# Kernel optimization log

Hardware: AMD Instinct MI355X
Metric: run time of the kernel (lower is better)

## Reference

```python
import jax, jax.numpy as jnp
import numpy as np

HEADS = 8
DIM_HEAD = 64
SCALE = DIM_HEAD ** -0.5


def setup_inputs() -> dict:
    key = jax.random.key(0)
    k1, k2, k3 = jax.random.split(key, 3)
    b, dim, n = 4, 256, 2048
    hidden = HEADS * DIM_HEAD  # 512
    x = jax.random.normal(k1, (b, dim, n), dtype=jnp.float32)
    # Conv1d kernel-size-1 weights are pointwise linear maps over channels.
    w_qkv = jax.random.normal(k2, (3 * hidden, dim), dtype=jnp.float32) * (dim ** -0.5)
    w_out = jax.random.normal(k3, (dim, hidden), dtype=jnp.float32) * (hidden ** -0.5)
    b_out = jnp.zeros((dim,), dtype=jnp.float32)
    return {"x": x, "w_qkv": w_qkv, "w_out": w_out, "b_out": b_out}


def reference(x, w_qkv, w_out, b_out):
    b, dim, n = x.shape
    hidden = w_out.shape[1]
    # pointwise conv1d == channel matmul: [3h, dim] x [b, dim, n] -> [b, 3h, n]
    qkv = jnp.einsum('oi,bin->bon', w_qkv, x)
    q, k, v = jnp.split(qkv, 3, axis=1)
    # b (h c) n -> b h c n
    reshape = lambda t: t.reshape(b, HEADS, DIM_HEAD, n)
    q, k, v = reshape(q) * SCALE, reshape(k), reshape(v)
    sim = jnp.einsum('bhdi,bhdj->bhij', q, k)          # [b, h, n, n]
    attn = jax.nn.softmax(sim, axis=-1)
    out = jnp.einsum('bhij,bhdj->bhid', attn, v)        # [b, h, n, d]
    # b h n d -> b (h d) n
    out = out.transpose(0, 1, 3, 2).reshape(b, hidden, n)
    return jnp.einsum('oi,bin->bon', w_out, out) + b_out[None, :, None]
```

## Files before the change

### kernel.cpp

```cpp
#include <hip/hip_runtime.h>
#include <stdint.h>

#define SEQ  2048
#define DIMC 256
#define HID  512
#define NH   8
#define DH   64

typedef __attribute__((ext_vector_type(8))) short bf16x8;
typedef __attribute__((ext_vector_type(4))) float f32x4;
typedef __attribute__((ext_vector_type(16))) float f32x16;
typedef __attribute__((ext_vector_type(2))) unsigned uint2v;
typedef __attribute__((address_space(1))) const uint32_t guint_t;
typedef __attribute__((address_space(3))) uint32_t luint_t;

__device__ __forceinline__ void gld16(const void* g, void* l) {
  __builtin_amdgcn_global_load_lds((guint_t*)g, (luint_t*)l, 16, 0, 0);
}

__device__ __forceinline__ void barrier_raw() {
  asm volatile("" ::: "memory");
  __builtin_amdgcn_s_barrier();
  asm volatile("" ::: "memory");
}
#define WAITVM(n) asm volatile("s_waitcnt vmcnt(" #n ")" ::: "memory")

__device__ __forceinline__ unsigned short f2bf(float f) {
  union { float f; uint32_t u; } v; v.f = f;
  return (unsigned short)((v.u + 0x7FFFu + ((v.u >> 16) & 1u)) >> 16);
}

__device__ __forceinline__ uint32_t fbits(float f) {
  union { float f; uint32_t u; } v; v.f = f; return v.u;
}
__device__ __forceinline__ float ffrombits(uint32_t u) {
  union { uint32_t u; float f; } v; v.u = u; return v.f;
}

__device__ __forceinline__ uint32_t cvtpk(float a, float b) {
  uint32_t r;
  asm("v_cvt_pk_bf16_f32 %0, %1, %2" : "=v"(r) : "v"(a), "v"(b));
  return r;
}

__device__ __forceinline__ void swap32(uint32_t& a, uint32_t& b) {
#if __has_builtin(__builtin_amdgcn_permlane32_swap)
  uint2v r = __builtin_amdgcn_permlane32_swap(a, b, false, false);
  a = r[0]; b = r[1];
#else
  uint32_t aw = __shfl_xor(a, 32);
  uint32_t bw = __shfl_xor(b, 32);
  bool lo = (threadIdx.x & 32) == 0;
  uint32_t an = lo ? a : bw;
  uint32_t bn = lo ? aw : b;
  a = an; b = bn;
#endif
}

__global__ __launch_bounds__(256) void prep_kernel(
    const float* __restrict__ x, const float* __restrict__ wqkv,
    const float* __restrict__ wout,
    unsigned short* __restrict__ wqkv_b, unsigned short* __restrict__ wout_b,
    unsigned short* __restrict__ xT) {
  __shared__ float tile[64][65];
  int blk = blockIdx.x;
  int t = threadIdx.x;
  if (blk < 384) {
    int idx = blk * 1024 + t * 4;
    float4 v = *(const float4*)(wqkv + idx);
    float s = ((idx >> 8) < HID) ? 0.18033688011112042f : 1.0f;
    ushort4 o;
    o.x = f2bf(v.x * s); o.y = f2bf(v.y * s);
    o.z = f2bf(v.z * s); o.w = f2bf(v.w * s);
    *(ushort4*)(wqkv_b + idx) = o;
    return;
  }
  if (blk < 512) {
    int idx = (blk - 384) * 1024 + t * 4;
    float4 v = *(const float4*)(wout + idx);
    ushort4 o;
    o.x = f2bf(v.x); o.y = f2bf(v.y); o.z = f2bf(v.z); o.w = f2bf(v.w);
    *(ushort4*)(wout_b + idx) = o;
    return;
  }
  int tid = blk - 512;
  int b  = tid >> 7;
  int r  = tid & 127;
  int i0 = (r >> 5) * 64;
  int n0 = (r & 31) * 64;
  const float* xb = x + (size_t)b * DIMC * SEQ;
  int tn = t & 15, ti = t >> 4;
#pragma unroll
  for (int j = 0; j < 4; j++) {
    int il = ti + j * 16;
    float4 v = *(const float4*)(xb + (size_t)(i0 + il) * SEQ + n0 + tn * 4);
    tile[il][tn*4+0] = v.x; tile[il][tn*4+1] = v.y;
    tile[il][tn*4+2] = v.z; tile[il][tn*4+3] = v.w;
  }
  __syncthreads();
  unsigned short* xTb = xT + (size_t)b * SEQ * DIMC;
#pragma unroll
  for (int j = 0; j < 4; j++) {
    int nl = ti + j * 16;
    int i4 = tn * 4;
    uint2 pk;
    pk.x = (uint32_t)f2bf(tile[i4+0][nl]) | ((uint32_t)f2bf(tile[i4+1][nl]) << 16);
    pk.y = (uint32_t)f2bf(tile[i4+2][nl]) | ((uint32_t)f2bf(tile[i4+3][nl]) << 16);
    *(uint2*)(xTb + (size_t)(n0 + nl) * DIMC + i0 + i4) = pk;
  }
}

__global__ __launch_bounds__(256, 3) void qkv_gemm(
    const unsigned short* __restrict__ wq, const unsigned short* __restrict__ xT,
    unsigned short* __restrict__ Qs, unsigned short* __restrict__ Ks,
    unsigned short* __restrict__ Vt) {
  __shared__ unsigned short lds[32768];
  int id = blockIdx.x + 12 * blockIdx.y + 192 * blockIdx.z;
  int xcd = id & 7, wg = id >> 3;
  int pair = xcd * 8 + wg / 12;
  int o0 = (wg % 12) * 128;
  int n0 = (pair & 15) * 128;
  int b  = pair >> 4;
  int t  = threadIdx.x;
  int wv = t >> 6, l = t & 63, l15 = l & 15, q = l >> 4;
  int wm = (wv & 1) * 64, wn = (wv >> 1) * 64;
  f32x4 acc[4][4];
#pragma unroll
  for (int i = 0; i < 4; i++)
#pragma unroll
    for (int j = 0; j < 4; j++) acc[i][j] = (f32x4){0.f, 0.f, 0.f, 0.f};
  const unsigned short* Ag = wq + (size_t)o0 * DIMC;
  const unsigned short* Bg = xT + ((size_t)b * SEQ + n0) * DIMC;
  int lrow8 = l >> 3, lcol = l & 7;

  auto stage = [&](int kk, int buf) {
    unsigned short* la = lds + (buf << 14);
    unsigned short* lb = la + 8192;
    int k0 = kk * 64;
#pragma unroll
    for (int c0 = 0; c0 < 4; c0++) {
      int c = wv * 4 + c0;
      int row = c * 8 + lrow8;
      int sg = lcol ^ (row & 7);
      gld16(Ag + (size_t)row * DIMC + k0 + sg * 8, la + c * 512);
      gld16(Bg + (size_t)row * DIMC + k0 + sg * 8, lb + c * 512);
    }
  };

  stage(0, 0);
  for (int kk = 0; kk < 4; kk++) {
    int cur = kk & 1;
    WAITVM(0);
    barrier_raw();
    if (kk < 3) stage(kk + 1, cur ^ 1);
    unsigned short* la = lds + (cur << 14);
    unsigned short* lb = la + 8192;
#pragma unroll
    for (int kh = 0; kh < 2; kh++) {
      bf16x8 af[4], bfr[4];
#pragma unroll
      for (int mt = 0; mt < 4; mt++) {
        int row = wm + mt*16 + l15;
        af[mt] = *(const bf16x8*)(la + row*64 + ((kh*4 + q) ^ (row & 7)) * 8);
      }
#pragma unroll
      for (int nt = 0; nt < 4; nt++) {
        int row = wn + nt*16 + l15;
        bfr[nt] = *(const bf16x8*)(lb + row*64 + ((kh*4 + q) ^ (row & 7)) * 8);
      }
#pragma unroll
      for (int mt = 0; mt < 4; mt++)
#pragma unroll
        for (int nt = 0; nt < 4; nt++)
          acc[mt][nt] = __builtin_amdgcn_mfma_f32_16x16x32_bf16(af[mt], bfr[nt], acc[mt][nt], 0, 0, 0);
    }
  }
  barrier_raw();
  int seg3 = o0 >> 9;
  int h0   = (o0 & 511) >> 6;
  if (seg3 == 2) {
#pragma unroll
    for (int mt = 0; mt < 4; mt++)
#pragma unroll
      for (int nt = 0; nt < 4; nt++)
#pragma unroll
        for (int r = 0; r < 4; r++) {
          int ol = wm + mt * 16 + q * 4 + r;
          int nn = wn + nt * 16 + l15;
          lds[ol * 136 + nn] = f2bf(acc[mt][nt][r]);
        }
    __syncthreads();
#pragma unroll
    for (int i = 0; i < 8; i++) {
      int idx = i * 256 + t;
      int ol  = idx >> 4;
      int nnb = (idx & 15) * 8;
      uint4 v = *(const uint4*)(lds + ol * 136 + nnb);
      int h = h0 + (ol >> 6), d = ol & 63;
      *(uint4*)(Vt + (((size_t)b * NH + h) * DH + d) * SEQ + n0 + nnb) = v;
    }
  } else {
    unsigned short* dst = (seg3 == 0) ? Qs : Ks;
#pragma unroll
    for (int mt = 0; mt < 4; mt++)
#pragma unroll
      for (int nt = 0; nt < 4; nt++)
#pragma unroll
        for (int r = 0; r < 4; r++) {
          int ol = wm + mt * 16 + q * 4 + r;
          int nn = wn + nt * 16 + l15;
          lds[nn * 136 + ol] = f2bf(acc[mt][nt][r]);
        }
    __syncthreads();
#pragma unroll
    for (int i = 0; i < 8; i++) {
      int idx = i * 256 + t;
      int nn  = idx >> 4;
      int olb = (idx & 15) * 8;
      uint4 v = *(const uint4*)(lds + nn * 136 + olb);
      int h = h0 + (olb >> 6), d = olb & 63;
      *(uint4*)(dst + (((size_t)b * NH + h) * SEQ + n0 + nn) * DH + d) = v;
    }
  }
}

__global__ __launch_bounds__(512, 4) void attn_kernel(
    const unsigned short* __restrict__ Qs, const unsigned short* __restrict__ Ks,
    const unsigned short* __restrict__ Vt, unsigned short* __restrict__ AO) {
  __shared__ unsigned short KVs[16384];
  __shared__ float Lc[256];
  int id = blockIdx.x;
  int s  = id >> 3;
  int bh = (id & 7) * 4 + (s & 3);
  int q0 = (s >> 2) * 128;
  int b = bh >> 3, h = bh & 7;
  int t = threadIdx.x;
  int w = t >> 6, l = t & 63, l31 = l & 31, lh = l >> 5;
  int cg = w & 1, qg = w >> 1;
  const unsigned short* Qg = Qs + ((size_t)bh * SEQ + q0 + qg * 32) * DH;
  bf16x8 qb[4];
#pragma unroll
  for (int kc = 0; kc < 4; kc++)
    qb[kc] = *(const bf16x8*)(Qg + l31 * DH + kc*16 + lh*8);
  f32x16 oacc[2];
  float lsum = 0.f;
#pragma unroll
  for (int dt = 0; dt < 2; dt++)
#pragma unroll
    for (int r = 0; r < 16; r++) oacc[dt][r] = 0.f;

  int which = w >> 1, half = w & 1;
  const unsigned short* sgp[2];
  unsigned short* dst0;
  size_t step;
  if (which < 2) {
    const unsigned short* Ksrc = Ks + ((size_t)bh * SEQ + which * 1024) * DH;
#pragma unroll
    for (int gi = 0; gi < 2; gi++) {
      int g = half * 2 + gi;
      int kr = g * 8 + (l >> 3);
      sgp[gi] = Ksrc + (size_t)kr * DH + ((l & 7) ^ (kr & 7)) * 8;
    }
    dst0 = (unsigned short*)KVs + which * 2048 + half * 1024;
    step = (size_t)32 * DH;
  } else {
    const unsigned short* Vsrc = Vt + (size_t)bh * DH * SEQ + (which - 2) * 1024;
#pragma unroll
    for (int gi = 0; gi < 2; gi++) {
      int g = half * 2 + gi;
      int r = g * 8 + (l >> 3);
      int u = (l & 7) ^ (r & 7);
      int d = (u >> 2) * 32 + r;
      int j = u & 3;
      sgp[gi] = Vsrc + (size_t)d * SEQ + j * 8;
    }
    dst0 = (unsigned short*)KVs + 4096 + (which - 2) * 2048 + half * 1024;
    step = 32;
  }

  auto stage = [&](int it2, int buf) {
    size_t off = (size_t)it2 * step;
    unsigned short* dstb = dst0 + buf * 8192;
    gld16(sgp[0] + off, dstb);
    gld16(sgp[1] + off, dstb + 512);
  };

  stage(0, 0);
  for (int it = 0; it < 32; it++) {
    int cur = it & 1;
    WAITVM(0);
    barrier_raw();
    if (it < 31) stage(it + 1, cur ^ 1);
    const unsigned short* Kst = KVs + cur * 8192 + cg * 2048;
    const unsigned short* Vst = KVs + cur * 8192 + 4096 + cg * 2048;
    f32x16 st;
#pragma unroll
    for (int r = 0; r < 16; r++) st[r] = 0.f;
    __builtin_amdgcn_s_setprio(1);
#pragma unroll
    for (int kc = 0; kc < 4; kc++) {
      bf16x8 kf = *(const bf16x8*)(Kst + l31 * 64 + ((kc*2 + lh) ^ (l31 & 7)) * 8);
      st = __builtin_amdgcn_mfma_f32_32x32x16_bf16(kf, qb[kc], st, 0, 0, 0);
    }
    __builtin_amdgcn_s_setprio(0);
    bf16x8 vf[2][2];
#pragma unroll
    for (int kc2 = 0; kc2 < 2; kc2++)
#pragma unroll
      for (int dt = 0; dt < 2; dt++)
        vf[kc2][dt] = *(const bf16x8*)(Vst + l31 * 64 +
                                       ((dt*4 + kc2*2 + lh) ^ (l31 & 7)) * 8);
    float p[16];
#pragma unroll
    for (int r = 0; r < 16; r++) p[r] = __builtin_amdgcn_exp2f(st[r]);
    {
      float t0=p[0]+p[1],  t1=p[2]+p[3],  t2=p[4]+p[5],   t3=p[6]+p[7];
      float t4=p[8]+p[9],  t5=p[10]+p[11], t6=p[12]+p[13], t7=p[14]+p[15];
      lsum += ((t0+t1)+(t2+t3)) + ((t4+t5)+(t6+t7));
    }
    bf16x8 af[2];
#pragma unroll
    for (int hf = 0; hf < 2; hf++) {
      uint32_t xs[4], ys[4];
#pragma unroll
      for (int j = 0; j < 4; j++) {
        xs[j] = fbits(p[hf*8 + j]);
        ys[j] = fbits(p[hf*8 + 4 + j]);
        swap32(xs[j], ys[j]);
      }
      union { uint32_t u[4]; bf16x8 v; } cv;
      cv.u[0] = cvtpk(ffrombits(xs[0]), ffrombits(xs[1]));
      cv.u[1] = cvtpk(ffrombits(xs[2]), ffrombits(xs[3]));
      cv.u[2] = cvtpk(ffrombits(ys[0]), ffrombits(ys[1]));
      cv.u[3] = cvtpk(ffrombits(ys[2]), ffrombits(ys[3]));
      af[hf] = cv.v;
    }
    __builtin_amdgcn_s_setprio(1);
#pragma unroll
    for (int kc2 = 0; kc2 < 2; kc2++)
#pragma unroll
      for (int dt = 0; dt < 2; dt++)
        oacc[dt] = __builtin_amdgcn_mfma_f32_32x32x16_bf16(af[kc2], vf[kc2][dt], oacc[dt], 0, 0, 0);
    __builtin_amdgcn_s_setprio(0);
  }
  {
    float v = lsum;
    v += __shfl_xor(v, 32);
    if (l < 32) Lc[cg * 128 + qg * 32 + l31] = v;
  }
  __syncthreads();
  float* Oc = (float*)KVs;
  if (cg == 1) {
#pragma unroll
    for (int dt = 0; dt < 2; dt++)
#pragma unroll
      for (int r = 0; r < 16; r++) {
        int qrow = qg*32 + (r & 3) + 8*(r >> 2) + 4*lh;
        Oc[qrow * 64 + dt*32 + l31] = oacc[dt][r];
      }
  }
  __syncthreads();
  if (cg == 0) {
    unsigned short* AOb = AO + (size_t)b * SEQ * HID + h * DH;
#pragma unroll
    for (int r = 0; r < 16; r++) {
      int qrow = qg*32 + (r & 3) + 8*(r >> 2) + 4*lh;
      float inv = __builtin_amdgcn_rcpf(Lc[qrow] + Lc[128 + qrow]);
      int n = q0 + qrow;
#pragma unroll
      for (int dt = 0; dt < 2; dt++) {
        float val = (oacc[dt][r] + Oc[qrow * 64 + dt*32 + l31]) * inv;
        AOb[(size_t)n * HID + dt*32 + l31] = f2bf(val);
      }
    }
  }
}

__global__ __launch_bounds__(256, 2) void out_gemm(
    const unsigned short* __restrict__ wo, const unsigned short* __restrict__ AO,
    const float* __restrict__ bias, float* __restrict__ out) {
  __shared__ unsigned short lds[16384];
  int id = blockIdx.x + 4 * blockIdx.y + 128 * blockIdx.z;
  int xcd = id & 7, wg = id >> 3;
  int pair = xcd * 16 + (wg >> 2);
  int o0 = (wg & 3) * 64;
  int n0 = (pair & 31) * 64;
  int b  = pair >> 5;
  int t  = threadIdx.x;
  int wv = t >> 6, l = t & 63, l15 = l & 15, q = l >> 4;
  int wm = (wv & 1) * 32, wn = (wv >> 1) * 32;
  f32x4 acc[2][2];
#pragma unroll
  for (int i = 0; i < 2; i++)
#pragma unroll
    for (int j = 0; j < 2; j++) acc[i][j] = (f32x4){0.f,0.f,0.f,0.f};
  const unsigned short* Ag = wo + (size_t)o0 * HID;
  const unsigned short* Bg = AO + ((size_t)b * SEQ + n0) * HID;
  int lrow8 = l >> 3, lcol = l & 7;

  auto stage = [&](int kk, int buf) {
    unsigned short* la = lds + buf * 8192;
    unsigned short* lb = la + 4096;
    int k0 = kk * 64;
#pragma unroll
    for (int c0 = 0; c0 < 2; c0++) {
      int c = wv * 2 + c0;
      int row = c * 8 + lrow8;
      int sg = lcol ^ (row & 7);
      gld16(Ag + (size_t)row * HID + k0 + sg * 8, la + c * 512);
      gld16(Bg + (size_t)row * HID + k0 + sg * 8, lb + c * 512);
    }
  };

  stage(0, 0);
  for (int kk = 0; kk < 8; kk++) {
    int cur = kk & 1;
    WAITVM(0);
    barrier_raw();
    if (kk < 7) stage(kk + 1, cur ^ 1);
    unsigned short* la = lds + cur * 8192;
    unsigned short* lb = la + 4096;
#pragma unroll
    for (int kh = 0; kh < 2; kh++) {
      bf16x8 af[2], bfr[2];
#pragma unroll
      for (int mt = 0; mt < 2; mt++) {
        int row = wm + mt*16 + l15;
        af[mt] = *(const bf16x8*)(la + row*64 + ((kh*4 + q) ^ (row & 7)) * 8);
      }
#pragma unroll
      for (int nt = 0; nt < 2; nt++) {
        int row = wn + nt*16 + l15;
        bfr[nt] = *(const bf16x8*)(lb + row*64 + ((kh*4 + q) ^ (row & 7)) * 8);
      }
#pragma unroll
      for (int mt = 0; mt < 2; mt++)
#pragma unroll
        for (int nt = 0; nt < 2; nt++)
          acc[mt][nt] = __builtin_amdgcn_mfma_f32_16x16x32_bf16(af[mt], bfr[nt], acc[mt][nt], 0,0,0);
    }
  }
#pragma unroll
  for (int mt = 0; mt < 2; mt++)
#pragma unroll
    for (int nt = 0; nt < 2; nt++)
#pragma unroll
      for (int r = 0; r < 4; r++) {
        int o2 = o0 + wm + mt*16 + q*4 + r;
        int n  = n0 + wn + nt*16 + l15;
        out[((size_t)b * DIMC + o2) * SEQ + n] = acc[mt][nt][r] + bias[o2];
      }
}

extern "C" void kernel_launch(void* const* d_in, const int* in_sizes, int n_in,
                              void* d_out, int out_size, void* d_ws, size_t ws_size,
                              hipStream_t stream) {
  const float* x    = (const float*)d_in[0];
  const float* wqkv = (const float*)d_in[1];
  const float* wout = (const float*)d_in[2];
  const float* bout = (const float*)d_in[3];
  float* out = (float*)d_out;
  char* ws = (char*)d_ws;
  unsigned short* wqkv_b = (unsigned short*)(ws);
  unsigned short* wout_b = (unsigned short*)(ws + 786432);
  unsigned short* xT     = (unsigned short*)(ws + 1048576);
  unsigned short* Qs     = (unsigned short*)(ws + 5242880);
  unsigned short* Ks     = (unsigned short*)(ws + 13631488);
  unsigned short* Vt     = (unsigned short*)(ws + 22020096);
  unsigned short* AO     = (unsigned short*)(ws + 30408704);
  prep_kernel<<<1024, 256, 0, stream>>>(x, wqkv, wout, wqkv_b, wout_b, xT);
  qkv_gemm<<<dim3(12, 16, 4), 256, 0, stream>>>(wqkv_b, xT, Qs, Ks, Vt);
  attn_kernel<<<512, 512, 0, stream>>>(Qs, Ks, Vt, AO);
  out_gemm<<<dim3(4, 32, 4), 256, 0, stream>>>(wout_b, AO, bout, out);
}
```

Before: 130.1 us.

## Split attention keys four ways per block, halve query tile, double grid

The attention kernel now handles 64 queries per block instead of 128 and splits the key range into four chunks of 512 keys, one per column group, instead of two. The grid doubles to 1024 blocks and the launch-bounds occupancy hint rises from 4 to 8. The double-buffered LDS staging is replaced by single-buffered loads with a barrier after each iteration, and partial outputs are combined through LDS in three serial reduction steps. The aim is more parallelism and occupancy, at the cost of losing load/compute overlap within a block, adding barriers, and making each query tile's Q reload more expensive.

Measured after the change: 453.2 us. 3.48x slower.

```diff
diff --git a/kernel.cpp b/kernel.cpp
--- a/kernel.cpp
+++ b/kernel.cpp
@@ -29,20 +29,17 @@
   union { float f; uint32_t u; } v; v.f = f;
   return (unsigned short)((v.u + 0x7FFFu + ((v.u >> 16) & 1u)) >> 16);
 }
-
 __device__ __forceinline__ uint32_t fbits(float f) {
   union { float f; uint32_t u; } v; v.f = f; return v.u;
 }
 __device__ __forceinline__ float ffrombits(uint32_t u) {
   union { uint32_t u; float f; } v; v.u = u; return v.f;
 }
-
 __device__ __forceinline__ uint32_t cvtpk(float a, float b) {
   uint32_t r;
   asm("v_cvt_pk_bf16_f32 %0, %1, %2" : "=v"(r) : "v"(a), "v"(b));
   return r;
 }
-
 __device__ __forceinline__ void swap32(uint32_t& a, uint32_t& b) {
 #if __has_builtin(__builtin_amdgcn_permlane32_swap)
   uint2v r = __builtin_amdgcn_permlane32_swap(a, b, false, false);
@@ -224,7 +221,7 @@
   }
 }
 
-__global__ __launch_bounds__(512, 4) void attn_kernel(
+__global__ __launch_bounds__(512, 8) void attn_kernel(
     const unsigned short* __restrict__ Qs, const unsigned short* __restrict__ Ks,
     const unsigned short* __restrict__ Vt, unsigned short* __restrict__ AO) {
   __shared__ unsigned short KVs[16384];
@@ -232,11 +229,11 @@
   int id = blockIdx.x;
   int s  = id >> 3;
   int bh = (id & 7) * 4 + (s & 3);
-  int q0 = (s >> 2) * 128;
+  int q0 = (s >> 2) * 64;
   int b = bh >> 3, h = bh & 7;
   int t = threadIdx.x;
   int w = t >> 6, l = t & 63, l31 = l & 31, lh = l >> 5;
-  int cg = w & 1, qg = w >> 1;
+  int cg = w & 3, qg = w >> 2;
   const unsigned short* Qg = Qs + ((size_t)bh * SEQ + q0 + qg * 32) * DH;
   bf16x8 qb[4];
 #pragma unroll
@@ -249,50 +246,37 @@
 #pragma unroll
     for (int r = 0; r < 16; r++) oacc[dt][r] = 0.f;
 
-  int which = w >> 1, half = w & 1;
-  const unsigned short* sgp[2];
-  unsigned short* dst0;
-  size_t step;
-  if (which < 2) {
-    const unsigned short* Ksrc = Ks + ((size_t)bh * SEQ + which * 1024) * DH;
-#pragma unroll
-    for (int gi = 0; gi < 2; gi++) {
-      int g = half * 2 + gi;
-      int kr = g * 8 + (l >> 3);
-      sgp[gi] = Ksrc + (size_t)kr * DH + ((l & 7) ^ (kr & 7)) * 8;
-    }
-    dst0 = (unsigned short*)KVs + which * 2048 + half * 1024;
+  int schunk = w >> 1, part = w & 1;
+  const unsigned short* sbase;
+  size_t gstride, step;
+  unsigned short* dstp;
+  if (part == 0) {
+    const unsigned short* Ksrc = Ks + ((size_t)bh * SEQ + schunk * 512) * DH;
+    int kr = l >> 3;
+    sbase = Ksrc + (size_t)kr * DH + ((l & 7) ^ (kr & 7)) * 8;
+    gstride = (size_t)8 * DH;
     step = (size_t)32 * DH;
+    dstp = (unsigned short*)KVs + schunk * 4096;
   } else {
-    const unsigned short* Vsrc = Vt + (size_t)bh * DH * SEQ + (which - 2) * 1024;
-#pragma unroll
-    for (int gi = 0; gi < 2; gi++) {
-      int g = half * 2 + gi;
-      int r = g * 8 + (l >> 3);
-      int u = (l & 7) ^ (r & 7);
-      int d = (u >> 2) * 32 + r;
-      int j = u & 3;
-      sgp[gi] = Vsrc + (size_t)d * SEQ + j * 8;
-    }
-    dst0 = (unsigned short*)KVs + 4096 + (which - 2) * 2048 + half * 1024;
+    const unsigned short* Vsrc = Vt + (size_t)bh * DH * SEQ + schunk * 512;
+    int r0 = l >> 3;
+    int u  = (l & 7) ^ (r0 & 7);
+    sbase = Vsrc + (size_t)((u >> 2) * 32 + r0) * SEQ + (u & 3) * 8;
+    gstride = (size_t)8 * SEQ;
     step = 32;
-  }
-
-  auto stage = [&](int it2, int buf) {
-    size_t off = (size_t)it2 * step;
-    unsigned short* dstb = dst0 + buf * 8192;
-    gld16(sgp[0] + off, dstb);
-    gld16(sgp[1] + off, dstb + 512);
-  };
-
-  stage(0, 0);
-  for (int it = 0; it < 32; it++) {
-    int cur = it & 1;
+    dstp = (unsigned short*)KVs + schunk * 4096 + 2048;
+  }
+
+  const unsigned short* Kst = KVs + cg * 4096;
+  const unsigned short* Vst = Kst + 2048;
+
+  for (int it = 0; it < 16; it++) {
+    const unsigned short* sp = sbase + (size_t)it * step;
+#pragma unroll
+    for (int g = 0; g < 4; g++)
+      gld16(sp + (size_t)g * gstride, dstp + g * 512);
     WAITVM(0);
     barrier_raw();
-    if (it < 31) stage(it + 1, cur ^ 1);
-    const unsigned short* Kst = KVs + cur * 8192 + cg * 2048;
-    const unsigned short* Vst = KVs + cur * 8192 + 4096 + cg * 2048;
     f32x16 st;
 #pragma unroll
     for (int r = 0; r < 16; r++) st[r] = 0.f;
@@ -342,15 +326,13 @@
       for (int dt = 0; dt < 2; dt++)
         oacc[dt] = __builtin_amdgcn_mfma_f32_32x32x16_bf16(af[kc2], vf[kc2][dt], oacc[dt], 0, 0, 0);
     __builtin_amdgcn_s_setprio(0);
-  }
-  {
-    float v = lsum;
-    v += __shfl_xor(v, 32);
-    if (l < 32) Lc[cg * 128 + qg * 32 + l31] = v;
-  }
+    barrier_raw();
+  }
+  lsum += __shfl_xor(lsum, 32);
+  if (l < 32) Lc[cg * 64 + qg * 32 + l31] = lsum;
   __syncthreads();
   float* Oc = (float*)KVs;
-  if (cg == 1) {
+  if (cg == 3) {
 #pragma unroll
     for (int dt = 0; dt < 2; dt++)
 #pragma unroll
@@ -360,12 +342,33 @@
       }
   }
   __syncthreads();
+  if (cg == 2) {
+#pragma unroll
+    for (int dt = 0; dt < 2; dt++)
+#pragma unroll
+      for (int r = 0; r < 16; r++) {
+        int qrow = qg*32 + (r & 3) + 8*(r >> 2) + 4*lh;
+        Oc[qrow * 64 + dt*32 + l31] += oacc[dt][r];
+      }
+  }
+  __syncthreads();
+  if (cg == 1) {
+#pragma unroll
+    for (int dt = 0; dt < 2; dt++)
+#pragma unroll
+      for (int r = 0; r < 16; r++) {
+        int qrow = qg*32 + (r & 3) + 8*(r >> 2) + 4*lh;
+        Oc[qrow * 64 + dt*32 + l31] += oacc[dt][r];
+      }
+  }
+  __syncthreads();
   if (cg == 0) {
     unsigned short* AOb = AO + (size_t)b * SEQ * HID + h * DH;
 #pragma unroll
     for (int r = 0; r < 16; r++) {
       int qrow = qg*32 + (r & 3) + 8*(r >> 2) + 4*lh;
-      float inv = __builtin_amdgcn_rcpf(Lc[qrow] + Lc[128 + qrow]);
+      float inv = __builtin_amdgcn_rcpf(Lc[qrow] + Lc[64 + qrow] +
+                                        Lc[128 + qrow] + Lc[192 + qrow]);
       int n = q0 + qrow;
 #pragma unroll
       for (int dt = 0; dt < 2; dt++) {
@@ -470,6 +473,6 @@
   unsigned short* AO     = (unsigned short*)(ws + 30408704);
   prep_kernel<<<1024, 256, 0, stream>>>(x, wqkv, wout, wqkv_b, wout_b, xT);
   qkv_gemm<<<dim3(12, 16, 4), 256, 0, stream>>>(wqkv_b, xT, Qs, Ks, Vt);
-  attn_kernel<<<512, 512, 0, stream>>>(Qs, Ks, Vt, AO);
+  attn_kernel<<<1024, 512, 0, stream>>>(Qs, Ks, Vt, AO);
   out_gemm<<<dim3(4, 32, 4), 256, 0, stream>>>(wout_b, AO, bout, out);
 }
```
